# Kernel optimization log

Measured on AMD Instinct MI355X. Metric: run time of the kernel, lower is better.

The kernel has to match this reference:

```python
import jax, jax.numpy as jnp
import numpy as np

BS = 128
E4M3_MAX = 448.0
E5M2_MAX = 57344.0


def qdq(x, fmax, dt):
    # block-wise (128-wide, last dim) fp8 quantize + dequantize (simulates act_quant + dequant in fp8_gemm)
    *lead, K = x.shape
    xb = x.reshape(*lead, K // BS, BS)
    s = jnp.maximum(jnp.max(jnp.abs(xb), axis=-1, keepdims=True) / fmax, 1e-12)
    xq = (xb / s).astype(dt).astype(jnp.float32)
    return (xq * s).reshape(*lead, K)


def fp8_linear(x, w, w_scale, fmax, dt, bias=None):
    # weight is fp8-valued (stored as f32 of the rounded values) with per-output-row-block scales
    x_dq = qdq(x, fmax, dt)
    sv = jnp.repeat(w_scale, BS)[: w.shape[0]]
    y = jnp.einsum('btk,ok->bto', x_dq, w * sv[:, None])
    return y if bias is None else y + bias


def fp8_ln(x, g, gs, b, bsc, eps=1e-5):
    mean = jnp.mean(x, axis=-1, keepdims=True)
    var = jnp.mean(jnp.square(x - mean), axis=-1, keepdims=True)  # unbiased=False
    xn = (x - mean) / jnp.sqrt(var + eps)
    d = x.shape[-1]
    return xn * (g * jnp.repeat(gs, BS)[:d]) + (b * jnp.repeat(bsc, BS)[:d])


def _fwd(x, attn_mask, wq, qs, wk, ks, wv, vs, wo, os_, fc1_w, fc1_s, fc1_b, fc2_w, fc2_s, fc2_b,
         ln1_g, ln1_gs, ln1_b, ln1_bs, ln2_g, ln2_gs, ln2_b, ln2_bs):
    B, T, C = x.shape
    H = 16
    HD = C // H
    e5 = jnp.float8_e5m2
    # attention (q/k/v/out projections use E5M2 fp8)
    q = fp8_linear(x, wq, qs, E5M2_MAX, e5).reshape(B, T, H, HD).transpose(0, 2, 1, 3)
    k = fp8_linear(x, wk, ks, E5M2_MAX, e5).reshape(B, T, H, HD).transpose(0, 2, 1, 3)
    v = fp8_linear(x, wv, vs, E5M2_MAX, e5).reshape(B, T, H, HD).transpose(0, 2, 1, 3)
    scores = jnp.einsum('bhqd,bhkd->bhqk', q, k) / jnp.sqrt(jnp.float32(HD))
    scores = jnp.where(attn_mask[:, None] == 0, -jnp.inf, scores)
    attn = jax.nn.softmax(scores, axis=-1)  # dropout = identity (eval)
    ctx = jnp.einsum('bhqk,bhkd->bhqd', attn, v).transpose(0, 2, 1, 3).reshape(B, T, C)
    attn_out = fp8_linear(ctx, wo, os_, E5M2_MAX, e5)
    x = fp8_ln(x + attn_out, ln1_g, ln1_gs, ln1_b, ln1_bs)
    # MLP (E4M3 fp8)
    e4 = jnp.float8_e4m3fn
    h = fp8_linear(x, fc1_w, fc1_s, E4M3_MAX, e4, fc1_b)
    h = jax.nn.gelu(h, approximate=False)  # torch nn.GELU default = exact erf
    ffn = fp8_linear(h, fc2_w, fc2_s, E4M3_MAX, e4, fc2_b)
    x = fp8_ln(x + ffn, ln2_g, ln2_gs, ln2_b, ln2_bs)
    return x


def _xavier_fp8(key, out_f, in_f, dt):
    bound = float(np.sqrt(6.0 / (in_f + out_f)))
    w = jax.random.uniform(key, (out_f, in_f), jnp.float32, -bound, bound)
    return w.astype(dt).astype(jnp.float32)  # simulate fp8 storage


def setup_inputs() -> dict:
    key = jax.random.key(0)
    kk = jax.random.split(key, 8)
    B, T, C, MLP = 2, 1024, 2048, 8192
    e5, e4 = jnp.float8_e5m2, jnp.float8_e4m3fn
    x = jax.random.normal(kk[0], (B, T, C), jnp.float32)
    attn_mask = jnp.broadcast_to(jnp.tril(jnp.ones((T, T), jnp.int32))[None], (B, T, T))
    nb = C // BS  # 16
    inp = {
        'x': x,
        'attn_mask': attn_mask,
        'wq': _xavier_fp8(kk[1], C, C, e5), 'qs': jnp.ones(nb, jnp.float32),
        'wk': _xavier_fp8(kk[2], C, C, e5), 'ks': jnp.ones(nb, jnp.float32),
        'wv': _xavier_fp8(kk[3], C, C, e5), 'vs': jnp.ones(nb, jnp.float32),
        'wo': _xavier_fp8(kk[4], C, C, e5), 'os_': jnp.ones(nb, jnp.float32),
        'fc1_w': _xavier_fp8(kk[5], MLP, C, e4), 'fc1_s': jnp.ones(MLP // BS, jnp.float32), 'fc1_b': jnp.zeros(MLP, jnp.float32),
        'fc2_w': _xavier_fp8(kk[6], C, MLP, e4), 'fc2_s': jnp.ones(nb, jnp.float32), 'fc2_b': jnp.zeros(C, jnp.float32),
        'ln1_g': jnp.ones(C, jnp.float32), 'ln1_gs': jnp.ones(nb, jnp.float32),
        'ln1_b': jnp.zeros(C, jnp.float32), 'ln1_bs': jnp.ones(nb, jnp.float32),
        'ln2_g': jnp.ones(C, jnp.float32), 'ln2_gs': jnp.ones(nb, jnp.float32),
        'ln2_b': jnp.zeros(C, jnp.float32), 'ln2_bs': jnp.ones(nb, jnp.float32),
    }
    return inp


def reference(x, attn_mask, wq, qs, wk, ks, wv, vs, wo, os_, fc1_w, fc1_s, fc1_b, fc2_w, fc2_s, fc2_b,
              ln1_g, ln1_gs, ln1_b, ln1_bs, ln2_g, ln2_gs, ln2_b, ln2_bs):
    return _fwd(x, attn_mask, wq, qs, wk, ks, wv, vs, wo, os_, fc1_w, fc1_s, fc1_b, fc2_w, fc2_s, fc2_b,
                ln1_g, ln1_gs, ln1_b, ln1_bs, ln2_g, ln2_gs, ln2_b, ln2_bs)
```

## Files before the change

kernel.cpp:

```cpp
#include <hip/hip_runtime.h>
#include <cstdint>


typedef __bf16 bf16x8 __attribute__((ext_vector_type(8)));
typedef unsigned short u16x8 __attribute__((ext_vector_type(8)));
typedef float f32x4 __attribute__((ext_vector_type(4)));
typedef float f32x16 __attribute__((ext_vector_type(16)));
typedef unsigned short u16;

#if __has_builtin(__builtin_amdgcn_exp2f)
#define EXP2F(x) __builtin_amdgcn_exp2f(x)
#else
#define EXP2F(x) exp2f(x)
#endif

__device__ __forceinline__ void gl_lds16(const void* g, void* l) {
  __builtin_amdgcn_global_load_lds(
      (const __attribute__((address_space(1))) void*)g,
      (__attribute__((address_space(3))) void*)l, 16, 0, 0);
}

__device__ __forceinline__ u16 bf16_rne(float v) {
  uint32_t u = __float_as_uint(v);
  u += 0x7FFFu + ((u >> 16) & 1u);
  return (u16)(u >> 16);
}

__device__ __forceinline__ float fp8_round(float v, int mbits, float minnorm, float subq) {
  float av = fabsf(v);
  if (av < minnorm) {
    return rintf(v / subq) * subq;
  }
  uint32_t u = __float_as_uint(v);
  const int shift = 23 - mbits;
  const uint32_t mask = (1u << shift) - 1u;
  const uint32_t rem = u & mask;
  uint32_t base = u & ~mask;
  const uint32_t half = 1u << (shift - 1);
  if (rem > half || (rem == half && ((base >> shift) & 1u))) base += (1u << shift);
  return __uint_as_float(base);
}

__global__ __launch_bounds__(256) void qdq_kernel(
    const float* __restrict__ x, u16* __restrict__ q, float* __restrict__ sT,
    int nblk, int kbshift, float fmax, float minnorm, float subq, int mbits) {
  const int wid = blockIdx.x * 4 + (threadIdx.x >> 6);
  if (wid >= nblk) return;
  const int lane = threadIdx.x & 63;
  const size_t base = (size_t)wid * 128 + (size_t)lane * 2;
  float2 v = *(const float2*)(x + base);
  float am = fmaxf(fabsf(v.x), fabsf(v.y));
#pragma unroll
  for (int m = 32; m >= 1; m >>= 1) am = fmaxf(am, __shfl_xor(am, m));
  const float sc = fmaxf(am / fmax, 1e-12f);
  const float q0 = fp8_round(v.x / sc, mbits, minnorm, subq);
  const float q1 = fp8_round(v.y / sc, mbits, minnorm, subq);
  ushort2 o;
  o.x = (u16)(__float_as_uint(q0) >> 16);
  o.y = (u16)(__float_as_uint(q1) >> 16);
  *(ushort2*)(q + base) = o;
  if (lane == 0) {
    const int kbs = 1 << kbshift;
    const int m = wid >> kbshift;
    const int kb = wid & (kbs - 1);
    sT[(size_t)kb * (nblk >> kbshift) + m] = sc;
  }
}

__global__ __launch_bounds__(256) void f32_to_bf16_kernel(
    const float* __restrict__ in, u16* __restrict__ out, int n4) {
  const int i = blockIdx.x * 256 + threadIdx.x;
  if (i >= n4) return;
  float4 v = ((const float4*)in)[i];
  ushort4 o;
  o.x = (u16)(__float_as_uint(v.x) >> 16);
  o.y = (u16)(__float_as_uint(v.y) >> 16);
  o.z = (u16)(__float_as_uint(v.z) >> 16);
  o.w = (u16)(__float_as_uint(v.w) >> 16);
  ((ushort4*)out)[i] = o;
}

__global__ void concat3_kernel(const float* __restrict__ a, const float* __restrict__ b,
                               const float* __restrict__ c, float* __restrict__ o, int n) {
  const int i = threadIdx.x;
  if (i < n) { o[i] = a[i]; o[n + i] = b[i]; o[2 * n + i] = c[i]; }
}

__global__ __launch_bounds__(256) void split_bf16_kernel(
    const float* __restrict__ in, u16* __restrict__ hi, u16* __restrict__ lo, int n4) {
  const int i = blockIdx.x * 256 + threadIdx.x;
  if (i >= n4) return;
  float4 v = ((const float4*)in)[i];
  float f[4] = {v.x, v.y, v.z, v.w};
  ushort4 oh, ol;
  u16* ph = (u16*)&oh;
  u16* pl = (u16*)&ol;
#pragma unroll
  for (int j = 0; j < 4; ++j) {
    u16 h = bf16_rne(f[j]);
    float hf = __uint_as_float((uint32_t)h << 16);
    ph[j] = h;
    pl[j] = bf16_rne(f[j] - hf);
  }
  ((ushort4*)hi)[i] = oh;
  ((ushort4*)lo)[i] = ol;
}

__global__ __launch_bounds__(256) void vtrans_kernel(
    const float* __restrict__ v, u16* __restrict__ vth, u16* __restrict__ vtl) {
  __shared__ float tile[64][65];
  const int tid = threadIdx.x;
  const int t0 = blockIdx.x * 64;
  const int d0 = blockIdx.y * 64;
  const int bh = blockIdx.z;
  const int b = bh >> 4, h = bh & 15;
#pragma unroll
  for (int s = 0; s < 4; ++s) {
    const int e = s * 256 + tid;
    const int r = e >> 4, c4 = e & 15;
    float4 val = *(const float4*)(v + ((size_t)(b * 1024 + t0 + r)) * 2048 + h * 128 + d0 + c4 * 4);
    tile[r][c4 * 4 + 0] = val.x;
    tile[r][c4 * 4 + 1] = val.y;
    tile[r][c4 * 4 + 2] = val.z;
    tile[r][c4 * 4 + 3] = val.w;
  }
  __syncthreads();
#pragma unroll
  for (int s = 0; s < 4; ++s) {
    const int e = s * 256 + tid;
    const int dr = e >> 4, tc4 = e & 15;
    ushort4 oh, ol;
    u16* ph = (u16*)&oh;
    u16* pl = (u16*)&ol;
#pragma unroll
    for (int i = 0; i < 4; ++i) {
      float f = tile[tc4 * 4 + i][dr];
      u16 hv = bf16_rne(f);
      ph[i] = hv;
      pl[i] = bf16_rne(f - __uint_as_float((uint32_t)hv << 16));
    }
    const size_t ob = ((size_t)(bh * 128 + d0 + dr)) * 1024 + t0 + tc4 * 4;
    *(ushort4*)(vth + ob) = oh;
    *(ushort4*)(vtl + ob) = ol;
  }
}

__global__ __launch_bounds__(256, 2) void attn_wave_kernel(
    const float* __restrict__ Q, const u16* __restrict__ Kh, const u16* __restrict__ Kl,
    const u16* __restrict__ Vth, const u16* __restrict__ Vtl, float* __restrict__ Octx) {
  constexpr int PLD = 34;
  __shared__ uint32_t Psm[4][32 * PLD];
  __shared__ float Osum[32 * 128];
  __shared__ float lsh[4][32];

  const int tid = threadIdx.x;
  const int w = tid >> 6;
  const int lane = tid & 63;
  const int l31 = lane & 31;
  const int q2 = lane >> 5;
  const int bh = blockIdx.x;
  const int b = bh >> 4;
  const int hofs = (bh & 15) * 128;
  const int qt = 31 - (int)blockIdx.y;
  const int i0 = qt * 32;
  const float SC2 = 0.12752698f;

  bf16x8 qh[8], ql[8];
  {
    const float* qp = Q + ((size_t)(b * 1024 + i0 + l31)) * 2048 + hofs + q2 * 8;
#pragma unroll
    for (int c = 0; c < 8; ++c) {
      float4 v0 = *(const float4*)(qp + c * 16);
      float4 v1 = *(const float4*)(qp + c * 16 + 4);
      float f[8] = {v0.x, v0.y, v0.z, v0.w, v1.x, v1.y, v1.z, v1.w};
      u16x8 uh, ul;
#pragma unroll
      for (int j = 0; j < 8; ++j) {
        u16 hv = bf16_rne(f[j]);
        uh[j] = hv;
        ul[j] = bf16_rne(f[j] - __uint_as_float((uint32_t)hv << 16));
      }
      qh[c] = __builtin_bit_cast(bf16x8, uh);
      ql[c] = __builtin_bit_cast(bf16x8, ul);
    }
  }

  const f32x16 z16 = {0.f};
  f32x16 Oacc[4] = {z16, z16, z16, z16};
  float lr[16];
#pragma unroll
  for (int r = 0; r < 16; ++r) lr[r] = 0.f;
  int rowq[16];
#pragma unroll
  for (int r = 0; r < 16; ++r) rowq[r] = (r & 3) + 8 * (r >> 2) + 4 * q2;

  uint32_t* Pw = Psm[w];
  for (int kt = w; kt <= qt; kt += 4) {
    const int j0 = kt * 32;
    const size_t krow = ((size_t)(b * 1024 + j0 + l31)) * 2048 + hofs + q2 * 8;
    f32x16 S = z16;
#pragma unroll
    for (int c = 0; c < 8; ++c) {
      bf16x8 k8h = *(const bf16x8*)(Kh + krow + c * 16);
      bf16x8 k8l = *(const bf16x8*)(Kl + krow + c * 16);
      S = __builtin_amdgcn_mfma_f32_32x32x16_bf16(qh[c], k8h, S, 0, 0, 0);
      S = __builtin_amdgcn_mfma_f32_32x32x16_bf16(qh[c], k8l, S, 0, 0, 0);
      S = __builtin_amdgcn_mfma_f32_32x32x16_bf16(ql[c], k8h, S, 0, 0, 0);
    }
    if (kt == qt) {
#pragma unroll
      for (int r = 0; r < 16; ++r)
        if (l31 > rowq[r]) S[r] = -3e38f;
    }
#pragma unroll
    for (int r = 0; r < 16; ++r) {
      const float p = EXP2F(S[r] * SC2);
      lr[r] += p;
      const u16 ph = bf16_rne(p);
      const u16 pl = bf16_rne(p - __uint_as_float((uint32_t)ph << 16));
      Pw[rowq[r] * PLD + l31] = (uint32_t)ph | ((uint32_t)pl << 16);
    }
#pragma unroll
    for (int s = 0; s < 2; ++s) {
      const uint32_t* rp = Pw + l31 * PLD + s * 16 + q2 * 8;
      uint2 a0 = *(const uint2*)(rp + 0);
      uint2 a1 = *(const uint2*)(rp + 2);
      uint2 a2 = *(const uint2*)(rp + 4);
      uint2 a3 = *(const uint2*)(rp + 6);
      u16x8 uh, ul;
      uh[0] = (u16)a0.x; ul[0] = (u16)(a0.x >> 16);
      uh[1] = (u16)a0.y; ul[1] = (u16)(a0.y >> 16);
      uh[2] = (u16)a1.x; ul[2] = (u16)(a1.x >> 16);
      uh[3] = (u16)a1.y; ul[3] = (u16)(a1.y >> 16);
      uh[4] = (u16)a2.x; ul[4] = (u16)(a2.x >> 16);
      uh[5] = (u16)a2.y; ul[5] = (u16)(a2.y >> 16);
      uh[6] = (u16)a3.x; ul[6] = (u16)(a3.x >> 16);
      uh[7] = (u16)a3.y; ul[7] = (u16)(a3.y >> 16);
      bf16x8 p8h = __builtin_bit_cast(bf16x8, uh);
      bf16x8 p8l = __builtin_bit_cast(bf16x8, ul);
      const size_t vrow = ((size_t)(bh * 128 + l31)) * 1024 + j0 + s * 16 + q2 * 8;
#pragma unroll
      for (int dt = 0; dt < 4; ++dt) {
        bf16x8 v8h = *(const bf16x8*)(Vth + vrow + (size_t)dt * 32768);
        bf16x8 v8l = *(const bf16x8*)(Vtl + vrow + (size_t)dt * 32768);
        Oacc[dt] = __builtin_amdgcn_mfma_f32_32x32x16_bf16(p8h, v8h, Oacc[dt], 0, 0, 0);
        Oacc[dt] = __builtin_amdgcn_mfma_f32_32x32x16_bf16(p8h, v8l, Oacc[dt], 0, 0, 0);
        Oacc[dt] = __builtin_amdgcn_mfma_f32_32x32x16_bf16(p8l, v8h, Oacc[dt], 0, 0, 0);
      }
    }
  }

#pragma unroll
  for (int r = 0; r < 16; ++r) {
    float t = lr[r];
    t += __shfl_xor(t, 1);
    t += __shfl_xor(t, 2);
    t += __shfl_xor(t, 4);
    t += __shfl_xor(t, 8);
    t += __shfl_xor(t, 16);
    lr[r] = t;
  }
  if (l31 == 0) {
#pragma unroll
    for (int r = 0; r < 16; ++r) lsh[w][rowq[r]] = lr[r];
  }
  if (w == 0) {
#pragma unroll
    for (int dt = 0; dt < 4; ++dt)
#pragma unroll
      for (int r = 0; r < 16; ++r) Osum[rowq[r] * 128 + dt * 32 + l31] = Oacc[dt][r];
  }
  __syncthreads();
  if (w == 1) {
#pragma unroll
    for (int dt = 0; dt < 4; ++dt)
#pragma unroll
      for (int r = 0; r < 16; ++r) Osum[rowq[r] * 128 + dt * 32 + l31] += Oacc[dt][r];
  }
  __syncthreads();
  if (w == 2) {
#pragma unroll
    for (int dt = 0; dt < 4; ++dt)
#pragma unroll
      for (int r = 0; r < 16; ++r) Osum[rowq[r] * 128 + dt * 32 + l31] += Oacc[dt][r];
  }
  __syncthreads();
  if (w == 3) {
#pragma unroll
    for (int dt = 0; dt < 4; ++dt)
#pragma unroll
      for (int r = 0; r < 16; ++r) Osum[rowq[r] * 128 + dt * 32 + l31] += Oacc[dt][r];
  }
  __syncthreads();
  const int row = w * 8 + (lane >> 3);
  const int c0 = (lane & 7) * 16;
  const float inv = 1.0f / (lsh[0][row] + lsh[1][row] + lsh[2][row] + lsh[3][row]);
  float* op = Octx + ((size_t)(b * 1024 + i0 + row)) * 2048 + hofs + c0;
#pragma unroll
  for (int i2 = 0; i2 < 4; ++i2) {
    float4 v = *(const float4*)(Osum + row * 128 + c0 + i2 * 4);
    v.x *= inv; v.y *= inv; v.z *= inv; v.w *= inv;
    *(float4*)(op + i2 * 4) = v;
  }
}

__global__ __launch_bounds__(256, 2) void gemm_bt_kernel(
    const u16* __restrict__ A, const float* __restrict__ sxT,
    const u16* __restrict__ W, const float* __restrict__ wsc,
    const float* __restrict__ bias, float* __restrict__ out,
    int M, int N, int K, int gelu, int seg_shift, int Nw) {
  __shared__ u16 As[128 * 64];
  __shared__ u16 Ws[128 * 64];
  const int tid = threadIdx.x;
  const int lane = tid & 63;
  const int wave = tid >> 6;
  const int wm = (wave >> 1) * 64;
  const int wn = (wave & 1) * 64;
  const int c16 = lane & 15;
  const int quad = lane >> 4;
  const int bm = blockIdx.y * 128;
  const int bn = blockIdx.x * 128;

  const int srow = wave * 8 + (lane >> 3);
  const int gchunk = (lane & 7) ^ (lane >> 3);
  const u16* ga = A + (size_t)(bm + srow) * K + gchunk * 8;
  const u16* gw = W + (size_t)(bn + srow) * K + gchunk * 8;
  u16* la = As + srow * 64 + (lane & 7) * 8;
  u16* lw = Ws + srow * 64 + (lane & 7) * 8;

  const f32x4 z = {0.f, 0.f, 0.f, 0.f};
  f32x4 acc[4][4], chk[4][4];
#pragma unroll
  for (int i = 0; i < 4; ++i)
#pragma unroll
    for (int j = 0; j < 4; ++j) { acc[i][j] = z; chk[i][j] = z; }

  const int nk = K >> 6;
  for (int kt = 0; kt < nk; ++kt) {
    __syncthreads();
#pragma unroll
    for (int s = 0; s < 4; ++s) {
      gl_lds16(ga + (size_t)s * 32 * K, la + s * 2048);
      gl_lds16(gw + (size_t)s * 32 * K, lw + s * 2048);
    }
    ga += 64;
    gw += 64;
    __syncthreads();
#pragma unroll
    for (int c = 0; c < 2; ++c) {
      bf16x8 af[4], bw[4];
#pragma unroll
      for (int i = 0; i < 4; ++i) {
        const int row = wm + i * 16 + c16;
        af[i] = *(const bf16x8*)(As + row * 64 + (((c * 4 + quad) ^ (c16 & 7)) * 8));
      }
#pragma unroll
      for (int j = 0; j < 4; ++j) {
        const int row = wn + j * 16 + c16;
        bw[j] = *(const bf16x8*)(Ws + row * 64 + (((c * 4 + quad) ^ (c16 & 7)) * 8));
      }
#pragma unroll
      for (int i = 0; i < 4; ++i)
#pragma unroll
        for (int j = 0; j < 4; ++j)
          chk[i][j] = __builtin_amdgcn_mfma_f32_16x16x32_bf16(af[i], bw[j], chk[i][j], 0, 0, 0);
    }
    if (kt & 1) {
      const int kb = kt >> 1;
#pragma unroll
      for (int i = 0; i < 4; ++i) {
        const f32x4 sv = *(const f32x4*)(sxT + (size_t)kb * M + bm + wm + i * 16 + quad * 4);
#pragma unroll
        for (int j = 0; j < 4; ++j) {
#pragma unroll
          for (int r = 0; r < 4; ++r) acc[i][j][r] += sv[r] * chk[i][j][r];
          chk[i][j] = z;
        }
      }
    }
  }
#pragma unroll
  for (int i = 0; i < 4; ++i) {
#pragma unroll
    for (int j = 0; j < 4; ++j) {
      const int n = bn + wn + j * 16 + c16;
      const float wsn = wsc[n >> 7];
      const float bv = bias ? bias[n] : 0.f;
      const int seg = n >> seg_shift;
      const int col = n & ((1 << seg_shift) - 1);
      float* op = out + (size_t)seg * M * Nw + col;
#pragma unroll
      for (int r = 0; r < 4; ++r) {
        const int m = bm + wm + i * 16 + quad * 4 + r;
        float v = acc[i][j][r] * wsn + bv;
        if (gelu) v = 0.5f * v * (1.f + erff(v * 0.70710678118654752440f));
        op[(size_t)m * Nw] = v;
      }
    }
  }
}

__global__ __launch_bounds__(256) void ln_kernel(
    const float* __restrict__ a, const float* __restrict__ b2,
    const float* __restrict__ g, const float* __restrict__ gs,
    const float* __restrict__ bb, const float* __restrict__ bs,
    float* __restrict__ out, int C) {
  __shared__ float red[4];
  const int tid = threadIdx.x;
  const int row = blockIdx.x;
  const float* pa = a + (size_t)row * C;
  const float* pb = b2 + (size_t)row * C;
  float v[8];
  float sum = 0.f;
#pragma unroll
  for (int k = 0; k < 8; ++k) {
    const int c = tid + (k << 8);
    v[k] = pa[c] + pb[c];
    sum += v[k];
  }
#pragma unroll
  for (int m = 32; m >= 1; m >>= 1) sum += __shfl_xor(sum, m);
  if ((tid & 63) == 0) red[tid >> 6] = sum;
  __syncthreads();
  const float mean = (red[0] + red[1] + red[2] + red[3]) * (1.f / 2048.f);
  __syncthreads();
  float sq = 0.f;
#pragma unroll
  for (int k = 0; k < 8; ++k) {
    const float d = v[k] - mean;
    sq += d * d;
  }
#pragma unroll
  for (int m = 32; m >= 1; m >>= 1) sq += __shfl_xor(sq, m);
  if ((tid & 63) == 0) red[tid >> 6] = sq;
  __syncthreads();
  const float var = (red[0] + red[1] + red[2] + red[3]) * (1.f / 2048.f);
  const float inv = 1.0f / sqrtf(var + 1e-5f);
  float* po = out + (size_t)row * C;
#pragma unroll
  for (int k = 0; k < 8; ++k) {
    const int c = tid + (k << 8);
    po[c] = (v[k] - mean) * inv * (g[c] * gs[c >> 7]) + bb[c] * bs[c >> 7];
  }
}

extern "C" void kernel_launch(void* const* d_in, const int* in_sizes, int n_in,
                              void* d_out, int out_size, void* d_ws, size_t ws_size,
                              hipStream_t stream) {
  const int C = 2048, MLP = 8192;
  const int M = 2048;

  const float* x = (const float*)d_in[0];
  const float* wq = (const float*)d_in[2];
  const float* qs = (const float*)d_in[3];
  const float* wk = (const float*)d_in[4];
  const float* ks = (const float*)d_in[5];
  const float* wv = (const float*)d_in[6];
  const float* vs = (const float*)d_in[7];
  const float* wo = (const float*)d_in[8];
  const float* os_ = (const float*)d_in[9];
  const float* fc1_w = (const float*)d_in[10];
  const float* fc1_s = (const float*)d_in[11];
  const float* fc1_b = (const float*)d_in[12];
  const float* fc2_w = (const float*)d_in[13];
  const float* fc2_s = (const float*)d_in[14];
  const float* fc2_b = (const float*)d_in[15];
  const float* ln1_g = (const float*)d_in[16];
  const float* ln1_gs = (const float*)d_in[17];
  const float* ln1_b = (const float*)d_in[18];
  const float* ln1_bs = (const float*)d_in[19];
  const float* ln2_g = (const float*)d_in[20];
  const float* ln2_gs = (const float*)d_in[21];
  const float* ln2_b = (const float*)d_in[22];
  const float* ln2_bs = (const float*)d_in[23];

  char* ws = (char*)d_ws;
  const size_t o_Aq = 0;
  const size_t o_Wb = 33554432;
  const size_t o_sx = 67108864;
  const size_t o_ln1 = 67633152;
  const size_t o_q = 84410368;
  const size_t o_k = 101187584;
  const size_t o_v = 117964800;
  const size_t o_ctx = 134742016;
  const size_t o_attn = 151519232;
  const size_t o_h = o_q;
  const size_t o_ffn = o_attn;
  if (ws_size < 168296448ull) return;

  u16* Aq = (u16*)(ws + o_Aq);
  u16* Wb = (u16*)(ws + o_Wb);
  float* sx = (float*)(ws + o_sx);
  float* wsc3 = (float*)(ws + o_sx + 131072 * 2);
  float* ln1o = (float*)(ws + o_ln1);
  float* qb = (float*)(ws + o_q);
  float* kb = (float*)(ws + o_k);
  float* vb = (float*)(ws + o_v);
  float* ctx = (float*)(ws + o_ctx);
  float* attn_out = (float*)(ws + o_attn);
  float* hb = (float*)(ws + o_h);
  float* ffn = (float*)(ws + o_ffn);
  float* outp = (float*)d_out;
  u16* Kh = (u16*)(ws + o_Aq);
  u16* Kl = (u16*)(ws + o_Aq + 8388608);
  u16* Vth = (u16*)(ws + o_Aq + 16777216);
  u16* Vtl = (u16*)(ws + o_Aq + 25165824);

  const float E5_MAX = 57344.f, E5_MINN = 6.103515625e-05f, E5_SUBQ = 1.52587890625e-05f;
  const float E4_MAX = 448.f, E4_MINN = 0.015625f, E4_SUBQ = 0.001953125f;

  const dim3 blk(256);
  const int wc_qkv = (C * C / 4 + 255) / 256;
  const int wc_fc = (C * MLP / 4 + 255) / 256;

  qdq_kernel<<<M * (C / 128) / 4, blk, 0, stream>>>(x, Aq, sx, M * (C / 128), 4, E5_MAX, E5_MINN, E5_SUBQ, 2);
  f32_to_bf16_kernel<<<wc_qkv, blk, 0, stream>>>(wq, Wb, C * C / 4);
  f32_to_bf16_kernel<<<wc_qkv, blk, 0, stream>>>(wk, Wb + C * C, C * C / 4);
  f32_to_bf16_kernel<<<wc_qkv, blk, 0, stream>>>(wv, Wb + 2 * C * C, C * C / 4);
  concat3_kernel<<<1, 64, 0, stream>>>(qs, ks, vs, wsc3, C / 128);
  gemm_bt_kernel<<<dim3(3 * C / 128, M / 128), blk, 0, stream>>>(
      Aq, sx, Wb, wsc3, nullptr, qb, M, 3 * C, C, 0, 11, C);

  split_bf16_kernel<<<(M * C / 4 + 255) / 256, blk, 0, stream>>>(kb, Kh, Kl, M * C / 4);
  vtrans_kernel<<<dim3(16, 2, 32), blk, 0, stream>>>(vb, Vth, Vtl);
  attn_wave_kernel<<<dim3(32, 32), blk, 0, stream>>>(qb, Kh, Kl, Vth, Vtl, ctx);

  qdq_kernel<<<M * (C / 128) / 4, blk, 0, stream>>>(ctx, Aq, sx, M * (C / 128), 4, E5_MAX, E5_MINN, E5_SUBQ, 2);
  f32_to_bf16_kernel<<<wc_qkv, blk, 0, stream>>>(wo, Wb, C * C / 4);
  gemm_bt_kernel<<<dim3(C / 128, M / 128), blk, 0, stream>>>(
      Aq, sx, Wb, os_, nullptr, attn_out, M, C, C, 0, 30, C);

  ln_kernel<<<M, blk, 0, stream>>>(x, attn_out, ln1_g, ln1_gs, ln1_b, ln1_bs, ln1o, C);

  qdq_kernel<<<M * (C / 128) / 4, blk, 0, stream>>>(ln1o, Aq, sx, M * (C / 128), 4, E4_MAX, E4_MINN, E4_SUBQ, 3);
  f32_to_bf16_kernel<<<wc_fc, blk, 0, stream>>>(fc1_w, Wb, C * MLP / 4);
  gemm_bt_kernel<<<dim3(MLP / 128, M / 128), blk, 0, stream>>>(
      Aq, sx, Wb, fc1_s, fc1_b, hb, M, MLP, C, 1, 30, MLP);

  qdq_kernel<<<M * (MLP / 128) / 4, blk, 0, stream>>>(hb, Aq, sx, M * (MLP / 128), 6, E4_MAX, E4_MINN, E4_SUBQ, 3);
  f32_to_bf16_kernel<<<wc_fc, blk, 0, stream>>>(fc2_w, Wb, C * MLP / 4);
  gemm_bt_kernel<<<dim3(C / 128, M / 128), blk, 0, stream>>>(
      Aq, sx, Wb, fc2_s, fc2_b, ffn, M, C, MLP, 0, 30, C);

  ln_kernel<<<M, blk, 0, stream>>>(ln1o, ffn, ln2_g, ln2_gs, ln2_b, ln2_bs, outp, C);
}
```

Before: 807.3 us.

## Switch projection and MLP GEMMs from bf16 MFMA to native fp8 scaled MFMA

Activations and weights are now encoded as real fp8 bytes (E5M2 for the attention projections, E4M3 for the MLP) instead of bf16. The GEMM uses the 32x32x64 f8f6f4 scaled MFMA with 128-wide K tiles and applies the per-block activation scale once per K tile. This halves operand bytes in memory and LDS and doubles MFMA throughput per instruction. In exchange it adds a custom fp8 encoder whose subnormal and edge-case handling must match the reference rounding exactly, and a new accumulator register layout that has to be correct.

```diff
diff --git a/kernel.cpp b/kernel.cpp
--- a/kernel.cpp
+++ b/kernel.cpp
@@ -6,6 +6,7 @@
 typedef unsigned short u16x8 __attribute__((ext_vector_type(8)));
 typedef float f32x4 __attribute__((ext_vector_type(4)));
 typedef float f32x16 __attribute__((ext_vector_type(16)));
+typedef int i32x8 __attribute__((ext_vector_type(8)));
 typedef unsigned short u16;
 
 #if __has_builtin(__builtin_amdgcn_exp2f)
@@ -18,6 +19,12 @@
   __builtin_amdgcn_global_load_lds(
       (const __attribute__((address_space(1))) void*)g,
       (__attribute__((address_space(3))) void*)l, 16, 0, 0);
+}
+
+struct u4x2 { uint4 a, b; };
+__device__ __forceinline__ i32x8 pack8(uint4 lo, uint4 hi) {
+  u4x2 t{lo, hi};
+  return __builtin_bit_cast(i32x8, t);
 }
 
 __device__ __forceinline__ u16 bf16_rne(float v) {
@@ -41,9 +48,22 @@
   return __uint_as_float(base);
 }
 
+__device__ __forceinline__ uint8_t fp8_encode(float v, int mbits, int bias) {
+  uint32_t u = __float_as_uint(v);
+  uint32_t sign = (u >> 31) << 7;
+  if ((u & 0x7FFFFFFFu) == 0) return (uint8_t)sign;
+  int e = (int)((u >> 23) & 255u) - 127;
+  if (e >= 1 - bias) {
+    uint32_t mant = (u >> (23 - mbits)) & ((1u << mbits) - 1u);
+    return (uint8_t)(sign | ((uint32_t)(e + bias) << mbits) | mant);
+  }
+  float q = fabsf(v) * __uint_as_float((uint32_t)(127 + bias - 1 + mbits) << 23);
+  return (uint8_t)(sign | (uint32_t)q);
+}
+
 __global__ __launch_bounds__(256) void qdq_kernel(
-    const float* __restrict__ x, u16* __restrict__ q, float* __restrict__ sT,
-    int nblk, int kbshift, float fmax, float minnorm, float subq, int mbits) {
+    const float* __restrict__ x, uint8_t* __restrict__ q, float* __restrict__ sT,
+    int nblk, int kbshift, float fmax, float minnorm, float subq, int mbits, int bias) {
   const int wid = blockIdx.x * 4 + (threadIdx.x >> 6);
   if (wid >= nblk) return;
   const int lane = threadIdx.x & 63;
@@ -55,10 +75,10 @@
   const float sc = fmaxf(am / fmax, 1e-12f);
   const float q0 = fp8_round(v.x / sc, mbits, minnorm, subq);
   const float q1 = fp8_round(v.y / sc, mbits, minnorm, subq);
-  ushort2 o;
-  o.x = (u16)(__float_as_uint(q0) >> 16);
-  o.y = (u16)(__float_as_uint(q1) >> 16);
-  *(ushort2*)(q + base) = o;
+  uchar2 o;
+  o.x = fp8_encode(q0, mbits, bias);
+  o.y = fp8_encode(q1, mbits, bias);
+  *(uchar2*)(q + base) = o;
   if (lane == 0) {
     const int kbs = 1 << kbshift;
     const int m = wid >> kbshift;
@@ -67,17 +87,17 @@
   }
 }
 
-__global__ __launch_bounds__(256) void f32_to_bf16_kernel(
-    const float* __restrict__ in, u16* __restrict__ out, int n4) {
+__global__ __launch_bounds__(256) void w_to_fp8_kernel(
+    const float* __restrict__ in, uint8_t* __restrict__ out, int n4, int mbits, int bias) {
   const int i = blockIdx.x * 256 + threadIdx.x;
   if (i >= n4) return;
   float4 v = ((const float4*)in)[i];
-  ushort4 o;
-  o.x = (u16)(__float_as_uint(v.x) >> 16);
-  o.y = (u16)(__float_as_uint(v.y) >> 16);
-  o.z = (u16)(__float_as_uint(v.z) >> 16);
-  o.w = (u16)(__float_as_uint(v.w) >> 16);
-  ((ushort4*)out)[i] = o;
+  uchar4 o;
+  o.x = fp8_encode(v.x, mbits, bias);
+  o.y = fp8_encode(v.y, mbits, bias);
+  o.z = fp8_encode(v.z, mbits, bias);
+  o.w = fp8_encode(v.w, mbits, bias);
+  *(uchar4*)(out + (size_t)i * 4) = o;
 }
 
 __global__ void concat3_kernel(const float* __restrict__ a, const float* __restrict__ b,
@@ -304,95 +324,100 @@
   }
 }
 
-__global__ __launch_bounds__(256, 2) void gemm_bt_kernel(
-    const u16* __restrict__ A, const float* __restrict__ sxT,
-    const u16* __restrict__ W, const float* __restrict__ wsc,
+template <int FMT>
+__global__ __launch_bounds__(256, 2) void gemm_fp8_kernel(
+    const uint8_t* __restrict__ A, const float* __restrict__ sxT,
+    const uint8_t* __restrict__ W, const float* __restrict__ wsc,
     const float* __restrict__ bias, float* __restrict__ out,
     int M, int N, int K, int gelu, int seg_shift, int Nw) {
-  __shared__ u16 As[128 * 64];
-  __shared__ u16 Ws[128 * 64];
+  __shared__ uint8_t As[128 * 128];
+  __shared__ uint8_t Ws[128 * 128];
   const int tid = threadIdx.x;
   const int lane = tid & 63;
   const int wave = tid >> 6;
   const int wm = (wave >> 1) * 64;
   const int wn = (wave & 1) * 64;
-  const int c16 = lane & 15;
-  const int quad = lane >> 4;
+  const int l31 = lane & 31;
+  const int q2 = lane >> 5;
   const int bm = blockIdx.y * 128;
   const int bn = blockIdx.x * 128;
 
   const int srow = wave * 8 + (lane >> 3);
   const int gchunk = (lane & 7) ^ (lane >> 3);
-  const u16* ga = A + (size_t)(bm + srow) * K + gchunk * 8;
-  const u16* gw = W + (size_t)(bn + srow) * K + gchunk * 8;
-  u16* la = As + srow * 64 + (lane & 7) * 8;
-  u16* lw = Ws + srow * 64 + (lane & 7) * 8;
-
-  const f32x4 z = {0.f, 0.f, 0.f, 0.f};
-  f32x4 acc[4][4], chk[4][4];
-#pragma unroll
-  for (int i = 0; i < 4; ++i)
-#pragma unroll
-    for (int j = 0; j < 4; ++j) { acc[i][j] = z; chk[i][j] = z; }
-
-  const int nk = K >> 6;
+  const uint8_t* ga = A + (size_t)(bm + srow) * K + gchunk * 16;
+  const uint8_t* gw = W + (size_t)(bn + srow) * K + gchunk * 16;
+  uint8_t* la = As + srow * 128 + (lane & 7) * 16;
+  uint8_t* lw = Ws + srow * 128 + (lane & 7) * 16;
+
+  const f32x16 z16 = {0.f};
+  f32x16 acc[2][2] = {{z16, z16}, {z16, z16}};
+
+  const int nk = K >> 7;
   for (int kt = 0; kt < nk; ++kt) {
     __syncthreads();
 #pragma unroll
     for (int s = 0; s < 4; ++s) {
-      gl_lds16(ga + (size_t)s * 32 * K, la + s * 2048);
-      gl_lds16(gw + (size_t)s * 32 * K, lw + s * 2048);
-    }
-    ga += 64;
-    gw += 64;
+      gl_lds16(ga + (size_t)s * 32 * K, la + s * 4096);
+      gl_lds16(gw + (size_t)s * 32 * K, lw + s * 4096);
+    }
+    ga += 128;
+    gw += 128;
     __syncthreads();
-#pragma unroll
-    for (int c = 0; c < 2; ++c) {
-      bf16x8 af[4], bw[4];
-#pragma unroll
-      for (int i = 0; i < 4; ++i) {
-        const int row = wm + i * 16 + c16;
-        af[i] = *(const bf16x8*)(As + row * 64 + (((c * 4 + quad) ^ (c16 & 7)) * 8));
+    f32x16 chk[2][2] = {{z16, z16}, {z16, z16}};
+#pragma unroll
+    for (int mf = 0; mf < 2; ++mf) {
+      i32x8 af[2], bf2[2];
+      const int c = mf * 4 + q2 * 2;
+#pragma unroll
+      for (int i = 0; i < 2; ++i) {
+        const int r = wm + i * 32 + l31;
+        const uint8_t* Ar = As + r * 128;
+        const int s7 = r & 7;
+        af[i] = pack8(*(const uint4*)(Ar + ((c ^ s7) * 16)),
+                      *(const uint4*)(Ar + (((c + 1) ^ s7) * 16)));
       }
 #pragma unroll
-      for (int j = 0; j < 4; ++j) {
-        const int row = wn + j * 16 + c16;
-        bw[j] = *(const bf16x8*)(Ws + row * 64 + (((c * 4 + quad) ^ (c16 & 7)) * 8));
+      for (int j = 0; j < 2; ++j) {
+        const int r = wn + j * 32 + l31;
+        const uint8_t* Wr = Ws + r * 128;
+        const int s7 = r & 7;
+        bf2[j] = pack8(*(const uint4*)(Wr + ((c ^ s7) * 16)),
+                       *(const uint4*)(Wr + (((c + 1) ^ s7) * 16)));
       }
 #pragma unroll
-      for (int i = 0; i < 4; ++i)
-#pragma unroll
-        for (int j = 0; j < 4; ++j)
-          chk[i][j] = __builtin_amdgcn_mfma_f32_16x16x32_bf16(af[i], bw[j], chk[i][j], 0, 0, 0);
-    }
-    if (kt & 1) {
-      const int kb = kt >> 1;
-#pragma unroll
-      for (int i = 0; i < 4; ++i) {
-        const f32x4 sv = *(const f32x4*)(sxT + (size_t)kb * M + bm + wm + i * 16 + quad * 4);
-#pragma unroll
-        for (int j = 0; j < 4; ++j) {
-#pragma unroll
-          for (int r = 0; r < 4; ++r) acc[i][j][r] += sv[r] * chk[i][j][r];
-          chk[i][j] = z;
-        }
+      for (int i = 0; i < 2; ++i)
+#pragma unroll
+        for (int j = 0; j < 2; ++j)
+          chk[i][j] = __builtin_amdgcn_mfma_scale_f32_32x32x64_f8f6f4(
+              af[i], bf2[j], chk[i][j], FMT, FMT, 0, 0x7F7F7F7F, 0, 0x7F7F7F7F);
+    }
+#pragma unroll
+    for (int i = 0; i < 2; ++i) {
+#pragma unroll
+      for (int rg = 0; rg < 4; ++rg) {
+        const f32x4 sv = *(const f32x4*)(sxT + (size_t)kt * M + bm + wm + i * 32 + rg * 8 + q2 * 4);
+#pragma unroll
+        for (int j = 0; j < 2; ++j)
+#pragma unroll
+          for (int rr = 0; rr < 4; ++rr)
+            acc[i][j][rg * 4 + rr] += sv[rr] * chk[i][j][rg * 4 + rr];
       }
     }
   }
 #pragma unroll
-  for (int i = 0; i < 4; ++i) {
-#pragma unroll
-    for (int j = 0; j < 4; ++j) {
-      const int n = bn + wn + j * 16 + c16;
+  for (int i = 0; i < 2; ++i) {
+#pragma unroll
+    for (int j = 0; j < 2; ++j) {
+      const int n = bn + wn + j * 32 + l31;
       const float wsn = wsc[n >> 7];
       const float bv = bias ? bias[n] : 0.f;
       const int seg = n >> seg_shift;
       const int col = n & ((1 << seg_shift) - 1);
       float* op = out + (size_t)seg * M * Nw + col;
 #pragma unroll
-      for (int r = 0; r < 4; ++r) {
-        const int m = bm + wm + i * 16 + quad * 4 + r;
-        float v = acc[i][j][r] * wsn + bv;
+      for (int reg = 0; reg < 16; ++reg) {
+        const int m = bm + wm + i * 32 + (reg & 3) + 8 * (reg >> 2) + 4 * q2;
+        float v = acc[i][j][reg] * wsn + bv;
         if (gelu) v = 0.5f * v * (1.f + erff(v * 0.70710678118654752440f));
         op[(size_t)m * Nw] = v;
       }
@@ -488,10 +513,10 @@
   const size_t o_ffn = o_attn;
   if (ws_size < 168296448ull) return;
 
-  u16* Aq = (u16*)(ws + o_Aq);
-  u16* Wb = (u16*)(ws + o_Wb);
+  uint8_t* Aq = (uint8_t*)(ws + o_Aq);
+  uint8_t* Wb = (uint8_t*)(ws + o_Wb);
   float* sx = (float*)(ws + o_sx);
-  float* wsc3 = (float*)(ws + o_sx + 131072 * 2);
+  float* wsc3 = (float*)(ws + o_sx + 262144);
   float* ln1o = (float*)(ws + o_ln1);
   float* qb = (float*)(ws + o_q);
   float* kb = (float*)(ws + o_k);
@@ -513,33 +538,33 @@
   const int wc_qkv = (C * C / 4 + 255) / 256;
   const int wc_fc = (C * MLP / 4 + 255) / 256;
 
-  qdq_kernel<<<M * (C / 128) / 4, blk, 0, stream>>>(x, Aq, sx, M * (C / 128), 4, E5_MAX, E5_MINN, E5_SUBQ, 2);
-  f32_to_bf16_kernel<<<wc_qkv, blk, 0, stream>>>(wq, Wb, C * C / 4);
-  f32_to_bf16_kernel<<<wc_qkv, blk, 0, stream>>>(wk, Wb + C * C, C * C / 4);
-  f32_to_bf16_kernel<<<wc_qkv, blk, 0, stream>>>(wv, Wb + 2 * C * C, C * C / 4);
+  qdq_kernel<<<M * (C / 128) / 4, blk, 0, stream>>>(x, Aq, sx, M * (C / 128), 4, E5_MAX, E5_MINN, E5_SUBQ, 2, 15);
+  w_to_fp8_kernel<<<wc_qkv, blk, 0, stream>>>(wq, Wb, C * C / 4, 2, 15);
+  w_to_fp8_kernel<<<wc_qkv, blk, 0, stream>>>(wk, Wb + C * C, C * C / 4, 2, 15);
+  w_to_fp8_kernel<<<wc_qkv, blk, 0, stream>>>(wv, Wb + 2 * C * C, C * C / 4, 2, 15);
   concat3_kernel<<<1, 64, 0, stream>>>(qs, ks, vs, wsc3, C / 128);
-  gemm_bt_kernel<<<dim3(3 * C / 128, M / 128), blk, 0, stream>>>(
+  gemm_fp8_kernel<1><<<dim3(3 * C / 128, M / 128), blk, 0, stream>>>(
       Aq, sx, Wb, wsc3, nullptr, qb, M, 3 * C, C, 0, 11, C);
 
   split_bf16_kernel<<<(M * C / 4 + 255) / 256, blk, 0, stream>>>(kb, Kh, Kl, M * C / 4);
   vtrans_kernel<<<dim3(16, 2, 32), blk, 0, stream>>>(vb, Vth, Vtl);
   attn_wave_kernel<<<dim3(32, 32), blk, 0, stream>>>(qb, Kh, Kl, Vth, Vtl, ctx);
 
-  qdq_kernel<<<M * (C / 128) / 4, blk, 0, stream>>>(ctx, Aq, sx, M * (C / 128), 4, E5_MAX, E5_MINN, E5_SUBQ, 2);
-  f32_to_bf16_kernel<<<wc_qkv, blk, 0, stream>>>(wo, Wb, C * C / 4);
-  gemm_bt_kernel<<<dim3(C / 128, M / 128), blk, 0, stream>>>(
+  qdq_kernel<<<M * (C / 128) / 4, blk, 0, stream>>>(ctx, Aq, sx, M * (C / 128), 4, E5_MAX, E5_MINN, E5_SUBQ, 2, 15);
+  w_to_fp8_kernel<<<wc_qkv, blk, 0, stream>>>(wo, Wb, C * C / 4, 2, 15);
+  gemm_fp8_kernel<1><<<dim3(C / 128, M / 128), blk, 0, stream>>>(
       Aq, sx, Wb, os_, nullptr, attn_out, M, C, C, 0, 30, C);
 
   ln_kernel<<<M, blk, 0, stream>>>(x, attn_out, ln1_g, ln1_gs, ln1_b, ln1_bs, ln1o, C);
 
-  qdq_kernel<<<M * (C / 128) / 4, blk, 0, stream>>>(ln1o, Aq, sx, M * (C / 128), 4, E4_MAX, E4_MINN, E4_SUBQ, 3);
-  f32_to_bf16_kernel<<<wc_fc, blk, 0, stream>>>(fc1_w, Wb, C * MLP / 4);
-  gemm_bt_kernel<<<dim3(MLP / 128, M / 128), blk, 0, stream>>>(
+  qdq_kernel<<<M * (C / 128) / 4, blk, 0, stream>>>(ln1o, Aq, sx, M * (C / 128), 4, E4_MAX, E4_MINN, E4_SUBQ, 3, 7);
+  w_to_fp8_kernel<<<wc_fc, blk, 0, stream>>>(fc1_w, Wb, C * MLP / 4, 3, 7);
+  gemm_fp8_kernel<0><<<dim3(MLP / 128, M / 128), blk, 0, stream>>>(
       Aq, sx, Wb, fc1_s, fc1_b, hb, M, MLP, C, 1, 30, MLP);
 
-  qdq_kernel<<<M * (MLP / 128) / 4, blk, 0, stream>>>(hb, Aq, sx, M * (MLP / 128), 6, E4_MAX, E4_MINN, E4_SUBQ, 3);
-  f32_to_bf16_kernel<<<wc_fc, blk, 0, stream>>>(fc2_w, Wb, C * MLP / 4);
-  gemm_bt_kernel<<<dim3(C / 128, M / 128), blk, 0, stream>>>(
+  qdq_kernel<<<M * (MLP / 128) / 4, blk, 0, stream>>>(hb, Aq, sx, M * (MLP / 128), 6, E4_MAX, E4_MINN, E4_SUBQ, 3, 7);
+  w_to_fp8_kernel<<<wc_fc, blk, 0, stream>>>(fc2_w, Wb, C * MLP / 4, 3, 7);
+  gemm_fp8_kernel<0><<<dim3(C / 128, M / 128), blk, 0, stream>>>(
       Aq, sx, Wb, fc2_s, fc2_b, ffn, M, C, MLP, 0, 30, C);
 
   ln_kernel<<<M, blk, 0, stream>>>(ln1o, ffn, ln2_g, ln2_gs, ln2_b, ln2_bs, outp, C);
```

Measured after the change: 657.6 us. -18.5%, faster.
